# Kernel tuning notes

Measured on AMD Instinct MI355X. Metric: run time of the kernel, lower is better.

The kernel has to match this reference:

```python
import jax, jax.numpy as jnp
import numpy as np

N = 100000      # nodes
E = 1600000     # edges
F_IN = 64       # num_node_features
HID = 128       # hidden_channels
HEADS = 8       # heads in gat1
G = 1000        # number of graphs
EPS = 1e-5


def _layer_norm(x, gamma, beta):
    mu = jnp.mean(x, axis=-1, keepdims=True)
    var = jnp.var(x, axis=-1, keepdims=True)
    return (x - mu) * jax.lax.rsqrt(var + EPS) * gamma + beta


def _gat_conv(x, src, dst, W, a_src, a_dst, b):
    # PyG GATConv (concat=True, negative_slope=0.2, self-loops already in src/dst)
    n = x.shape[0]
    heads, c = a_src.shape
    h = (x @ W).reshape(n, heads, c)                      # [N,H,C]
    alpha_s = jnp.sum(h * a_src[None], axis=-1)           # [N,H]
    alpha_d = jnp.sum(h * a_dst[None], axis=-1)           # [N,H]
    e = jax.nn.leaky_relu(alpha_s[src] + alpha_d[dst], 0.2)   # [Etot,H]
    m = jax.ops.segment_max(e, dst, num_segments=n)       # per-dst max (stable softmax)
    e = jnp.exp(e - m[dst])
    denom = jax.ops.segment_sum(e, dst, num_segments=n)
    attn = e / (denom[dst] + 1e-16)                        # [Etot,H]
    out = jax.ops.segment_sum(h[src] * attn[:, :, None], dst, num_segments=n)
    return out.reshape(n, heads * c) + b


def setup_inputs():
    key = jax.random.key(0)
    ks = jax.random.split(key, 32)
    s = 0.05
    inp = {
        'x': jax.random.normal(ks[0], (N, F_IN), dtype=jnp.float32),
        'edge_index': jax.random.randint(ks[1], (2, E), 0, N),
        'batch': jnp.sort(jax.random.randint(ks[2], (N,), 0, G)),
        # gat1: 64 -> 16 per head, 8 heads
        'W1': jax.random.normal(ks[3], (F_IN, HID), dtype=jnp.float32) * s,
        'as1': jax.random.normal(ks[4], (HEADS, HID // HEADS), dtype=jnp.float32) * s,
        'ad1': jax.random.normal(ks[5], (HEADS, HID // HEADS), dtype=jnp.float32) * s,
        'b1': jnp.zeros((HID,), dtype=jnp.float32),
        # gat2: 128 -> 128, 1 head
        'W2': jax.random.normal(ks[6], (HID, HID), dtype=jnp.float32) * s,
        'as2': jax.random.normal(ks[7], (1, HID), dtype=jnp.float32) * s,
        'ad2': jax.random.normal(ks[8], (1, HID), dtype=jnp.float32) * s,
        'b2': jnp.zeros((HID,), dtype=jnp.float32),
        # gat3
        'W3': jax.random.normal(ks[9], (HID, HID), dtype=jnp.float32) * s,
        'as3': jax.random.normal(ks[10], (1, HID), dtype=jnp.float32) * s,
        'ad3': jax.random.normal(ks[11], (1, HID), dtype=jnp.float32) * s,
        'b3': jnp.zeros((HID,), dtype=jnp.float32),
        # layer norms
        'g1': jnp.ones((HID,), dtype=jnp.float32), 'be1': jnp.zeros((HID,), dtype=jnp.float32),
        'g2': jnp.ones((HID,), dtype=jnp.float32), 'be2': jnp.zeros((HID,), dtype=jnp.float32),
        'g3': jnp.ones((HID,), dtype=jnp.float32), 'be3': jnp.zeros((HID,), dtype=jnp.float32),
        # linear heads
        'lw1': jax.random.normal(ks[12], (HID, HID), dtype=jnp.float32) * s,
        'lb1': jnp.zeros((HID,), dtype=jnp.float32),
        'lw2': jax.random.normal(ks[13], (HID, HID), dtype=jnp.float32) * s,
        'lb2': jnp.zeros((HID,), dtype=jnp.float32),
    }
    return inp


def reference(x, edge_index, batch, W1, as1, ad1, b1, W2, as2, ad2, b2,
              W3, as3, ad3, b3, g1, be1, g2, be2, g3, be3, lw1, lb1, lw2, lb2):
    n = x.shape[0]
    loops = jnp.arange(n)
    src = jnp.concatenate([edge_index[0], loops])   # add self-loops (PyG default)
    dst = jnp.concatenate([edge_index[1], loops])

    h = _gat_conv(x, src, dst, W1, as1, ad1, b1)
    h = _layer_norm(jax.nn.elu(h), g1, be1)          # dropout is identity in eval

    idn2 = h
    h = _gat_conv(h, src, dst, W2, as2, ad2, b2)
    h = _layer_norm(jax.nn.elu(h), g2, be2) + idn2

    idn3 = h
    h = _gat_conv(h, src, dst, W3, as3, ad3, b3)
    h = _layer_norm(jax.nn.elu(h), g3, be3) + idn3

    # global mean pool over graphs
    sums = jax.ops.segment_sum(h, batch, num_segments=G)
    cnt = jax.ops.segment_sum(jnp.ones((n, 1), h.dtype), batch, num_segments=G)
    pooled = sums / jnp.maximum(cnt, 1.0)

    out = jax.nn.elu(pooled @ lw1 + lb1)
    return out @ lw2 + lb2
```

## Files before the change

kernel.cpp:

```cpp
#include <hip/hip_runtime.h>
#include <hip/hip_bf16.h>
#include <cstdint>
#include <cstddef>

constexpr int F_IN = 64;
constexpr int HID  = 128;
constexpr int SCHUNK = 4096;

typedef __attribute__((ext_vector_type(8))) short short8v;
typedef __attribute__((ext_vector_type(4))) float f32x4;

__device__ __forceinline__ float bf2f(unsigned short u) {
  return __uint_as_float((unsigned)u << 16);
}
__device__ __forceinline__ unsigned short f2bf(float x) {
  unsigned u = __float_as_uint(x);
  u += 0x7FFFu + ((u >> 16) & 1u);
  return (unsigned short)(u >> 16);
}

__global__ __launch_bounds__(256) void k_bhist(const int* __restrict__ ei,
                                               int* __restrict__ bcnt, int E, int n) {
  __shared__ int hist[1024];
  int t = threadIdx.x;
  for (int k = t; k < 1024; k += 256) hist[k] = 0;
  __syncthreads();
  int tot = E + n;
  for (int i = blockIdx.x * 256 + t; i < tot; i += gridDim.x * 256) {
    int d = (i < E) ? ei[E + i] : (i - E);
    atomicAdd(&hist[d >> 7], 1);
  }
  __syncthreads();
  for (int k = t; k < 1024; k += 256)
    if (hist[k]) atomicAdd(&bcnt[k], hist[k]);
}

__global__ __launch_bounds__(1024) void k_bscan(const int* __restrict__ bcnt,
                                                int* __restrict__ boff,
                                                int* __restrict__ bcur, int nb) {
  __shared__ int tmp[1024];
  int t = threadIdx.x;
  int v = (t < nb) ? bcnt[t] : 0;
  tmp[t] = v;
  __syncthreads();
  #pragma unroll
  for (int off = 1; off < 1024; off <<= 1) {
    int x = tmp[t];
    int add = (t >= off) ? tmp[t - off] : 0;
    __syncthreads();
    tmp[t] = x + add;
    __syncthreads();
  }
  if (t < nb) {
    int ex = tmp[t] - v;
    boff[t] = ex;
    bcur[t] = ex;
    if (t == nb - 1) boff[nb] = tmp[t];
  }
}

__global__ __launch_bounds__(256) void k_bscat(const int* __restrict__ ei,
                                               int* __restrict__ bcur,
                                               uint2* __restrict__ pairs, int E, int n) {
  __shared__ int lh[1024];
  __shared__ int lc[1024];
  int t = threadIdx.x;
  int tot = E + n;
  int start = blockIdx.x * SCHUNK;
  if (start >= tot) return;
  int end = min(start + SCHUNK, tot);
  for (int k = t; k < 1024; k += 256) { lh[k] = 0; lc[k] = 0; }
  __syncthreads();
  int dreg[SCHUNK / 256];
  #pragma unroll
  for (int q = 0; q < SCHUNK / 256; ++q) {
    int i = start + q * 256 + t;
    int d = (i < end) ? ((i < E) ? ei[E + i] : (i - E)) : -1;
    dreg[q] = d;
    if (d >= 0) atomicAdd(&lh[d >> 7], 1);
  }
  __syncthreads();
  for (int k = t; k < 1024; k += 256) {
    int c = lh[k];
    lh[k] = (c > 0) ? atomicAdd(&bcur[k], c) : 0;
  }
  __syncthreads();
  #pragma unroll
  for (int q = 0; q < SCHUNK / 256; ++q) {
    int i = start + q * 256 + t;
    int d = dreg[q];
    if (d < 0) continue;
    int s = (i < E) ? ei[i] : (i - E);
    int b = d >> 7;
    int loc = atomicAdd(&lc[b], 1);
    pairs[lh[b] + loc] = make_uint2((unsigned)s, (unsigned)d);
  }
}

__global__ __launch_bounds__(256) void k_bfin(const uint2* __restrict__ pairs,
                                              const int* __restrict__ boff,
                                              int* __restrict__ row_off,
                                              int* __restrict__ csr_src,
                                              int n, int tot) {
  __shared__ int ldeg[128];
  __shared__ int lcur[128];
  int b = blockIdx.x;
  int t = threadIdx.x;
  int pb = boff[b], pe = boff[b + 1];
  if (t < 128) ldeg[t] = 0;
  __syncthreads();
  for (int j = pb + t; j < pe; j += 256)
    atomicAdd(&ldeg[pairs[j].y & 127], 1);
  __syncthreads();
  int cnt = (t < 128) ? ldeg[t] : 0;
  for (int off = 1; off < 128; off <<= 1) {
    int add = (t < 128 && t >= off) ? ldeg[t - off] : 0;
    __syncthreads();
    if (t < 128) ldeg[t] += add;
    __syncthreads();
  }
  if (t < 128) {
    int base = pb + ldeg[t] - cnt;
    lcur[t] = base;
    int idx = (b << 7) + t;
    if (idx < n) row_off[idx] = base;
  }
  if (b == 0 && t == 255) row_off[n] = tot;
  __syncthreads();
  for (int j = pb + t; j < pe; j += 256) {
    uint2 pr = pairs[j];
    int pos = atomicAdd(&lcur[pr.y & 127], 1);
    csr_src[pos] = (int)pr.x;
  }
}

__global__ void k_tobf(const float* __restrict__ X, unsigned short* __restrict__ Y,
                       int total) {
  int i = blockIdx.x * 256 + threadIdx.x;
  if (i < total) Y[i] = f2bf(X[i]);
}

__global__ void k_wpack(const float* __restrict__ W, unsigned short* __restrict__ Wf,
                        int K) {
  int i = blockIdx.x * 256 + threadIdx.x;
  int total = (K >> 5) * 4096;
  if (i >= total) return;
  int j    = i & 7;
  int lane = (i >> 3) & 63;
  int t    = (i >> 9) & 7;
  int ks   = i >> 12;
  int k = ks * 32 + (lane >> 4) * 8 + j;
  int c = t * 16 + (lane & 15);
  Wf[i] = f2bf(W[k * 128 + c]);
}

template<int K>
__global__ __launch_bounds__(256) void k_mgemm(const short* __restrict__ Xb,
                                               const short* __restrict__ Wf,
                                               unsigned short* __restrict__ Y, int n) {
  int wv   = threadIdx.x >> 6;
  int lane = threadIdx.x & 63;
  int r0   = blockIdx.x * 64 + wv * 16;
  int ln = lane & 15, kg = lane >> 4;
  f32x4 acc[8] = {};
  int arow = min(r0 + ln, n - 1);
  const short* aptr = Xb + arow * K + kg * 8;
  #pragma unroll
  for (int ks = 0; ks < K / 32; ++ks) {
    short8v a = *(const short8v*)(aptr + ks * 32);
    const short* wp = Wf + ks * 4096 + lane * 8;
    #pragma unroll
    for (int t = 0; t < 8; ++t) {
      short8v b = *(const short8v*)(wp + t * 512);
      acc[t] = __builtin_amdgcn_mfma_f32_16x16x32_bf16(a, b, acc[t], 0, 0, 0);
    }
  }
  #pragma unroll
  for (int t = 0; t < 8; ++t) {
    #pragma unroll
    for (int reg = 0; reg < 4; ++reg) {
      int r = r0 + kg * 4 + reg;
      if (r < n) Y[r * 128 + t * 16 + ln] = f2bf(acc[t][reg]);
    }
  }
}

template<int LOGC>
__global__ __launch_bounds__(256) void k_alpha(const unsigned short* __restrict__ H,
    const float* __restrict__ a_s, const float* __restrict__ a_d,
    float* __restrict__ AS, float* __restrict__ AD, int n) {
  int wid  = (int)((blockIdx.x * (size_t)blockDim.x + threadIdx.x) >> 6);
  int lane = threadIdx.x & 63;
  if (wid >= n) return;
  constexpr int SEG = 1 << (LOGC - 1);
  constexpr int NH  = HID >> LOGC;
  int c = 2 * lane;
  ushort2 u = *(const ushort2*)(H + wid * HID + c);
  float h0 = bf2f(u.x), h1 = bf2f(u.y);
  float s1 = h0 * a_s[c] + h1 * a_s[c + 1];
  float s2 = h0 * a_d[c] + h1 * a_d[c + 1];
  #pragma unroll
  for (int off = 1; off < SEG; off <<= 1) {
    s1 += __shfl_xor(s1, off);
    s2 += __shfl_xor(s2, off);
  }
  if ((lane & (SEG - 1)) == 0) {
    int h = lane / SEG;
    AS[wid * NH + h] = s1;
    AD[wid * NH + h] = s2;
  }
}

template<int LOGC>
__global__ __launch_bounds__(256) void k_agg_post(const unsigned short* __restrict__ Hu,
    const int* __restrict__ row_off, const int* __restrict__ csr_src,
    const float* __restrict__ AS, const float* __restrict__ AD,
    const float* __restrict__ bias, const float* __restrict__ RES,
    const float* __restrict__ gamma, const float* __restrict__ beta,
    float* __restrict__ Y, unsigned short* __restrict__ Yb, int n, int has_res) {
  int tid = blockIdx.x * 256 + threadIdx.x;
  int wid = tid >> 5;
  int ll  = threadIdx.x & 31;
  if (wid >= n) return;
  constexpr int NH  = HID >> LOGC;
  constexpr int SEG = (LOGC >= 7) ? 32 : (1 << (LOGC - 2));
  int abslane = threadIdx.x & 63;
  int c = ll << 2;
  int h = c >> LOGC;
  int r = ll & (SEG - 1);
  int sbase = abslane & ~(SEG - 1);
  float adv = AD[wid * NH + h];
  int jb = row_off[wid], je = row_off[wid + 1];
  float den = 0.f, a0 = 0.f, a1 = 0.f, a2 = 0.f, a3 = 0.f;
  for (int j0 = jb; j0 < je; j0 += SEG) {
    int cnt = min(SEG, je - j0);
    int s_l = 0; float p_l = 0.f;
    if (r < cnt) {
      s_l = csr_src[j0 + r];
      float e = AS[s_l * NH + h] + adv;
      e = (e > 0.f) ? e : 0.2f * e;
      p_l = __expf(e);
    }
    int k = 0;
    for (; k + 4 <= cnt; k += 4) {
      int sk0 = __shfl(s_l, sbase | k);
      int sk1 = __shfl(s_l, sbase | (k + 1));
      int sk2 = __shfl(s_l, sbase | (k + 2));
      int sk3 = __shfl(s_l, sbase | (k + 3));
      ushort4 u0 = *(const ushort4*)(Hu + (sk0 << 7) + c);
      ushort4 u1 = *(const ushort4*)(Hu + (sk1 << 7) + c);
      ushort4 u2 = *(const ushort4*)(Hu + (sk2 << 7) + c);
      ushort4 u3 = *(const ushort4*)(Hu + (sk3 << 7) + c);
      float p0 = __shfl(p_l, sbase | k);
      float p1 = __shfl(p_l, sbase | (k + 1));
      float p2 = __shfl(p_l, sbase | (k + 2));
      float p3 = __shfl(p_l, sbase | (k + 3));
      den += (p0 + p1) + (p2 + p3);
      a0 = fmaf(p0, bf2f(u0.x), a0); a1 = fmaf(p0, bf2f(u0.y), a1);
      a2 = fmaf(p0, bf2f(u0.z), a2); a3 = fmaf(p0, bf2f(u0.w), a3);
      a0 = fmaf(p1, bf2f(u1.x), a0); a1 = fmaf(p1, bf2f(u1.y), a1);
      a2 = fmaf(p1, bf2f(u1.z), a2); a3 = fmaf(p1, bf2f(u1.w), a3);
      a0 = fmaf(p2, bf2f(u2.x), a0); a1 = fmaf(p2, bf2f(u2.y), a1);
      a2 = fmaf(p2, bf2f(u2.z), a2); a3 = fmaf(p2, bf2f(u2.w), a3);
      a0 = fmaf(p3, bf2f(u3.x), a0); a1 = fmaf(p3, bf2f(u3.y), a1);
      a2 = fmaf(p3, bf2f(u3.z), a2); a3 = fmaf(p3, bf2f(u3.w), a3);
    }
    for (; k < cnt; ++k) {
      int   s  = __shfl(s_l, sbase | k);
      float pk = __shfl(p_l, sbase | k);
      ushort4 u = *(const ushort4*)(Hu + (s << 7) + c);
      den += pk;
      a0 = fmaf(pk, bf2f(u.x), a0); a1 = fmaf(pk, bf2f(u.y), a1);
      a2 = fmaf(pk, bf2f(u.z), a2); a3 = fmaf(pk, bf2f(u.w), a3);
    }
  }
  float inv = 1.f / (den + 1e-16f);
  float4 bv = *(const float4*)(bias + c);
  float t0 = a0 * inv + bv.x;
  float t1 = a1 * inv + bv.y;
  float t2 = a2 * inv + bv.z;
  float t3 = a3 * inv + bv.w;
  float e0 = t0 > 0.f ? t0 : __expf(t0) - 1.f;
  float e1 = t1 > 0.f ? t1 : __expf(t1) - 1.f;
  float e2 = t2 > 0.f ? t2 : __expf(t2) - 1.f;
  float e3 = t3 > 0.f ? t3 : __expf(t3) - 1.f;
  float s1 = (e0 + e1) + (e2 + e3);
  float s2 = (e0 * e0 + e1 * e1) + (e2 * e2 + e3 * e3);
  #pragma unroll
  for (int off = 16; off >= 1; off >>= 1) {
    s1 += __shfl_xor(s1, off);
    s2 += __shfl_xor(s2, off);
  }
  float mu  = s1 * (1.f / 128.f);
  float var = s2 * (1.f / 128.f) - mu * mu;
  float rs  = rsqrtf(var + 1e-5f);
  int base = wid * HID;
  float4 rv = make_float4(0.f, 0.f, 0.f, 0.f);
  if (has_res) rv = *(const float4*)(RES + base + c);
  float4 gv = *(const float4*)(gamma + c);
  float4 betv = *(const float4*)(beta + c);
  float4 o;
  o.x = (e0 - mu) * rs * gv.x + betv.x + rv.x;
  o.y = (e1 - mu) * rs * gv.y + betv.y + rv.y;
  o.z = (e2 - mu) * rs * gv.z + betv.z + rv.z;
  o.w = (e3 - mu) * rs * gv.w + betv.w + rv.w;
  *(float4*)(Y + base + c) = o;
  if (Yb) {
    ushort4 ob;
    ob.x = f2bf(o.x);
    ob.y = f2bf(o.y);
    ob.z = f2bf(o.z);
    ob.w = f2bf(o.w);
    *(ushort4*)(Yb + base + c) = ob;
  }
}

__global__ __launch_bounds__(256) void k_pool_seg(const float* __restrict__ Hf,
    const int* __restrict__ batch, float* __restrict__ pool, int n, int G) {
  int wid  = (int)((blockIdx.x * (size_t)blockDim.x + threadIdx.x) >> 6);
  int lane = threadIdx.x & 63;
  if (wid >= G) return;
  int lo = 0, hi = n;
  while (lo < hi) { int mid = (lo + hi) >> 1; if (batch[mid] < wid) lo = mid + 1; else hi = mid; }
  int start = lo;
  hi = n;
  while (lo < hi) { int mid = (lo + hi) >> 1; if (batch[mid] < wid + 1) lo = mid + 1; else hi = mid; }
  int end = lo;
  int c = 2 * lane;
  float s0 = 0.f, s1 = 0.f;
  for (int i = start; i < end; ++i) {
    float2 v = *(const float2*)(Hf + (size_t)i * HID + c);
    s0 += v.x; s1 += v.y;
  }
  float inv = 1.f / (float)max(end - start, 1);
  pool[(size_t)wid * HID + c]     = s0 * inv;
  pool[(size_t)wid * HID + c + 1] = s1 * inv;
}

__global__ void k_mlp(const float* __restrict__ X, const float* __restrict__ Wt,
                      const float* __restrict__ bb, float* __restrict__ Y,
                      int rows, int do_elu) {
  int i = blockIdx.x * blockDim.x + threadIdx.x;
  if (i >= rows * HID) return;
  int r = i >> 7, c = i & 127;
  const float* xr = X + (size_t)r * HID;
  float acc = bb[c];
  for (int k = 0; k < HID; ++k) acc += xr[k] * Wt[k * HID + c];
  if (do_elu) acc = acc > 0.f ? acc : __expf(acc) - 1.f;
  Y[i] = acc;
}

extern "C" void kernel_launch(void* const* d_in, const int* in_sizes, int n_in,
                              void* d_out, int out_size, void* d_ws, size_t ws_size,
                              hipStream_t stream) {
  const float* x   = (const float*)d_in[0];
  const int*   ei  = (const int*)d_in[1];
  const int*   bat = (const int*)d_in[2];
  const float* W1  = (const float*)d_in[3];
  const float* as1 = (const float*)d_in[4];
  const float* ad1 = (const float*)d_in[5];
  const float* b1  = (const float*)d_in[6];
  const float* W2  = (const float*)d_in[7];
  const float* as2 = (const float*)d_in[8];
  const float* ad2 = (const float*)d_in[9];
  const float* b2  = (const float*)d_in[10];
  const float* W3  = (const float*)d_in[11];
  const float* as3 = (const float*)d_in[12];
  const float* ad3 = (const float*)d_in[13];
  const float* b3  = (const float*)d_in[14];
  const float* g1  = (const float*)d_in[15];
  const float* be1 = (const float*)d_in[16];
  const float* g2  = (const float*)d_in[17];
  const float* be2 = (const float*)d_in[18];
  const float* g3  = (const float*)d_in[19];
  const float* be3 = (const float*)d_in[20];
  const float* lw1 = (const float*)d_in[21];
  const float* lb1 = (const float*)d_in[22];
  const float* lw2 = (const float*)d_in[23];
  const float* lb2 = (const float*)d_in[24];

  int N = in_sizes[0] / F_IN;
  int E = in_sizes[1] / 2;
  int G = out_size / HID;
  int tot = E + N;
  int nb  = (N + 127) >> 7;

  char* p = (char*)d_ws;
  auto alloc = [&](size_t bytes) { char* r = p; p += (bytes + 511) & ~(size_t)511; return r; };
  int*   bcnt    = (int*)  alloc(1024 * 4);
  int*   boff    = (int*)  alloc(1025 * 4);
  int*   bcur    = (int*)  alloc(1024 * 4);
  int*   row_off = (int*)  alloc((size_t)(N + 1) * 4);
  int*   csr_src = (int*)  alloc((size_t)tot * 4);
  uint2* pairs   = (uint2*)alloc((size_t)tot * 8);
  float* AS      = (float*)alloc((size_t)N * 8 * 4);
  float* AD      = (float*)alloc((size_t)N * 8 * 4);
  unsigned short* Hb  = (unsigned short*)alloc((size_t)N * HID * 2);
  unsigned short* Fb  = (unsigned short*)alloc((size_t)N * HID * 2);
  float* F0      = (float*)alloc((size_t)N * HID * 4);
  float* F1      = (float*)alloc((size_t)N * HID * 4);
  float* pool    = (float*)alloc((size_t)G * HID * 4);
  float* t1      = (float*)alloc((size_t)G * HID * 4);
  unsigned short* Wf1 = (unsigned short*)alloc(64 * 128 * 2);
  unsigned short* Wf2 = (unsigned short*)alloc(128 * 128 * 2);
  unsigned short* Wf3 = (unsigned short*)alloc(128 * 128 * 2);
  unsigned short* xb  = (unsigned short*)pairs;

  (void)hipMemsetAsync(bcnt, 0, 1024 * 4, stream);

  int sb = (tot + SCHUNK - 1) / SCHUNK;
  k_bhist<<<256, 256, 0, stream>>>(ei, bcnt, E, N);
  k_bscan<<<1, 1024, 0, stream>>>(bcnt, boff, bcur, nb);
  k_bscat<<<sb, 256, 0, stream>>>(ei, bcur, pairs, E, N);
  k_bfin <<<nb, 256, 0, stream>>>(pairs, boff, row_off, csr_src, N, tot);

  k_tobf <<<(N * F_IN + 255) / 256, 256, 0, stream>>>(x, xb, N * F_IN);
  k_wpack<<<(64 * 128 + 255) / 256, 256, 0, stream>>>(W1, Wf1, 64);
  k_wpack<<<(128 * 128 + 255) / 256, 256, 0, stream>>>(W2, Wf2, 128);
  k_wpack<<<(128 * 128 + 255) / 256, 256, 0, stream>>>(W3, Wf3, 128);

  int mb  = (N + 63) / 64;
  int nw  = (N + 3) / 4;
  int nh2 = (N + 7) / 8;

  k_mgemm<64><<<mb, 256, 0, stream>>>((const short*)xb, (const short*)Wf1, Hb, N);
  k_alpha<4><<<nw, 256, 0, stream>>>(Hb, as1, ad1, AS, AD, N);
  k_agg_post<4><<<nh2, 256, 0, stream>>>(Hb, row_off, csr_src, AS, AD, b1,
                                         nullptr, g1, be1, F0, Fb, N, 0);

  k_mgemm<128><<<mb, 256, 0, stream>>>((const short*)Fb, (const short*)Wf2, Hb, N);
  k_alpha<7><<<nw, 256, 0, stream>>>(Hb, as2, ad2, AS, AD, N);
  k_agg_post<7><<<nh2, 256, 0, stream>>>(Hb, row_off, csr_src, AS, AD, b2,
                                         F0, g2, be2, F1, Fb, N, 1);

  k_mgemm<128><<<mb, 256, 0, stream>>>((const short*)Fb, (const short*)Wf3, Hb, N);
  k_alpha<7><<<nw, 256, 0, stream>>>(Hb, as3, ad3, AS, AD, N);
  k_agg_post<7><<<nh2, 256, 0, stream>>>(Hb, row_off, csr_src, AS, AD, b3,
                                         F1, g3, be3, F0, nullptr, N, 1);

  k_pool_seg<<<(G + 3) / 4, 256, 0, stream>>>(F0, bat, pool, N, G);
  k_mlp<<<(G * HID + 255) / 256, 256, 0, stream>>>(pool, lw1, lb1, t1, G, 1);
  k_mlp<<<(G * HID + 255) / 256, 256, 0, stream>>>(t1, lw2, lb2, (float*)d_out, G, 0);
}
```

Before: 468.4 us.

## Fuse attention logits into GEMM, store activations as bf16, unroll aggregation by 8

The attention-coefficient dot products (alpha_src/alpha_dst) are now computed in the MFMA GEMM epilogue from the fp32 accumulators, which removes the separate k_alpha kernels and their re-read of H. Layer outputs, residuals and the pooling input are stored only as bf16 instead of both fp32 and bf16, cutting memory traffic in aggregation and pooling. The single-head aggregation loop also issues 8 gathers at a time to get more loads in flight. The trade-off is lower residual precision from bf16 storage and more register pressure in the GEMM epilogue and aggregation loop.

```diff
diff --git a/kernel.cpp b/kernel.cpp
--- a/kernel.cpp
+++ b/kernel.cpp
@@ -154,10 +154,14 @@
   Wf[i] = f2bf(W[k * 128 + c]);
 }
 
-template<int K>
+template<int K, int HEADS>
 __global__ __launch_bounds__(256) void k_mgemm(const short* __restrict__ Xb,
                                                const short* __restrict__ Wf,
-                                               unsigned short* __restrict__ Y, int n) {
+                                               const float* __restrict__ a_s,
+                                               const float* __restrict__ a_d,
+                                               unsigned short* __restrict__ Y,
+                                               float* __restrict__ AS,
+                                               float* __restrict__ AD, int n) {
   int wv   = threadIdx.x >> 6;
   int lane = threadIdx.x & 63;
   int r0   = blockIdx.x * 64 + wv * 16;
@@ -175,6 +179,50 @@
       acc[t] = __builtin_amdgcn_mfma_f32_16x16x32_bf16(a, b, acc[t], 0, 0, 0);
     }
   }
+  float asv[8], adv[8];
+  #pragma unroll
+  for (int t = 0; t < 8; ++t) { asv[t] = a_s[t * 16 + ln]; adv[t] = a_d[t * 16 + ln]; }
+  #pragma unroll
+  for (int reg = 0; reg < 4; ++reg) {
+    int r = r0 + kg * 4 + reg;
+    bool valid = (r < n);
+    if (HEADS == 1) {
+      float s1 = 0.f, s2 = 0.f;
+      #pragma unroll
+      for (int t = 0; t < 8; ++t) {
+        s1 = fmaf(acc[t][reg], asv[t], s1);
+        s2 = fmaf(acc[t][reg], adv[t], s2);
+      }
+      #pragma unroll
+      for (int off = 1; off < 16; off <<= 1) {
+        s1 += __shfl_xor(s1, off);
+        s2 += __shfl_xor(s2, off);
+      }
+      if (valid && ln == 0) { AS[r] = s1; AD[r] = s2; }
+    } else {
+      float s1[8], s2[8];
+      #pragma unroll
+      for (int t = 0; t < 8; ++t) {
+        s1[t] = acc[t][reg] * asv[t];
+        s2[t] = acc[t][reg] * adv[t];
+      }
+      #pragma unroll
+      for (int off = 1; off < 16; off <<= 1) {
+        #pragma unroll
+        for (int t = 0; t < 8; ++t) {
+          s1[t] += __shfl_xor(s1[t], off);
+          s2[t] += __shfl_xor(s2[t], off);
+        }
+      }
+      float w1 = s1[0], w2 = s2[0];
+      #pragma unroll
+      for (int t = 1; t < 8; ++t) {
+        w1 = (ln == t) ? s1[t] : w1;
+        w2 = (ln == t) ? s2[t] : w2;
+      }
+      if (valid && ln < 8) { AS[r * 8 + ln] = w1; AD[r * 8 + ln] = w2; }
+    }
+  }
   #pragma unroll
   for (int t = 0; t < 8; ++t) {
     #pragma unroll
@@ -186,38 +234,12 @@
 }
 
 template<int LOGC>
-__global__ __launch_bounds__(256) void k_alpha(const unsigned short* __restrict__ H,
-    const float* __restrict__ a_s, const float* __restrict__ a_d,
-    float* __restrict__ AS, float* __restrict__ AD, int n) {
-  int wid  = (int)((blockIdx.x * (size_t)blockDim.x + threadIdx.x) >> 6);
-  int lane = threadIdx.x & 63;
-  if (wid >= n) return;
-  constexpr int SEG = 1 << (LOGC - 1);
-  constexpr int NH  = HID >> LOGC;
-  int c = 2 * lane;
-  ushort2 u = *(const ushort2*)(H + wid * HID + c);
-  float h0 = bf2f(u.x), h1 = bf2f(u.y);
-  float s1 = h0 * a_s[c] + h1 * a_s[c + 1];
-  float s2 = h0 * a_d[c] + h1 * a_d[c + 1];
-  #pragma unroll
-  for (int off = 1; off < SEG; off <<= 1) {
-    s1 += __shfl_xor(s1, off);
-    s2 += __shfl_xor(s2, off);
-  }
-  if ((lane & (SEG - 1)) == 0) {
-    int h = lane / SEG;
-    AS[wid * NH + h] = s1;
-    AD[wid * NH + h] = s2;
-  }
-}
-
-template<int LOGC>
 __global__ __launch_bounds__(256) void k_agg_post(const unsigned short* __restrict__ Hu,
     const int* __restrict__ row_off, const int* __restrict__ csr_src,
     const float* __restrict__ AS, const float* __restrict__ AD,
-    const float* __restrict__ bias, const float* __restrict__ RES,
+    const float* __restrict__ bias, const unsigned short* __restrict__ RES,
     const float* __restrict__ gamma, const float* __restrict__ beta,
-    float* __restrict__ Y, unsigned short* __restrict__ Yb, int n, int has_res) {
+    unsigned short* __restrict__ Yb, int n, int has_res) {
   int tid = blockIdx.x * 256 + threadIdx.x;
   int wid = tid >> 5;
   int ll  = threadIdx.x & 31;
@@ -242,6 +264,25 @@
       p_l = __expf(e);
     }
     int k = 0;
+    if (LOGC >= 7) {
+      for (; k + 8 <= cnt; k += 8) {
+        int   sk[8]; float pk[8]; ushort4 uu[8];
+        #pragma unroll
+        for (int q = 0; q < 8; ++q) sk[q] = __shfl(s_l, sbase | (k + q));
+        #pragma unroll
+        for (int q = 0; q < 8; ++q) uu[q] = *(const ushort4*)(Hu + (sk[q] << 7) + c);
+        #pragma unroll
+        for (int q = 0; q < 8; ++q) pk[q] = __shfl(p_l, sbase | (k + q));
+        #pragma unroll
+        for (int q = 0; q < 8; ++q) {
+          den += pk[q];
+          a0 = fmaf(pk[q], bf2f(uu[q].x), a0);
+          a1 = fmaf(pk[q], bf2f(uu[q].y), a1);
+          a2 = fmaf(pk[q], bf2f(uu[q].z), a2);
+          a3 = fmaf(pk[q], bf2f(uu[q].w), a3);
+        }
+      }
+    }
     for (; k + 4 <= cnt; k += 4) {
       int sk0 = __shfl(s_l, sbase | k);
       int sk1 = __shfl(s_l, sbase | (k + 1));
@@ -295,27 +336,22 @@
   float var = s2 * (1.f / 128.f) - mu * mu;
   float rs  = rsqrtf(var + 1e-5f);
   int base = wid * HID;
-  float4 rv = make_float4(0.f, 0.f, 0.f, 0.f);
-  if (has_res) rv = *(const float4*)(RES + base + c);
+  float r0 = 0.f, r1 = 0.f, r2 = 0.f, r3 = 0.f;
+  if (has_res) {
+    ushort4 rv = *(const ushort4*)(RES + base + c);
+    r0 = bf2f(rv.x); r1 = bf2f(rv.y); r2 = bf2f(rv.z); r3 = bf2f(rv.w);
+  }
   float4 gv = *(const float4*)(gamma + c);
   float4 betv = *(const float4*)(beta + c);
-  float4 o;
-  o.x = (e0 - mu) * rs * gv.x + betv.x + rv.x;
-  o.y = (e1 - mu) * rs * gv.y + betv.y + rv.y;
-  o.z = (e2 - mu) * rs * gv.z + betv.z + rv.z;
-  o.w = (e3 - mu) * rs * gv.w + betv.w + rv.w;
-  *(float4*)(Y + base + c) = o;
-  if (Yb) {
-    ushort4 ob;
-    ob.x = f2bf(o.x);
-    ob.y = f2bf(o.y);
-    ob.z = f2bf(o.z);
-    ob.w = f2bf(o.w);
-    *(ushort4*)(Yb + base + c) = ob;
-  }
-}
-
-__global__ __launch_bounds__(256) void k_pool_seg(const float* __restrict__ Hf,
+  ushort4 ob;
+  ob.x = f2bf((e0 - mu) * rs * gv.x + betv.x + r0);
+  ob.y = f2bf((e1 - mu) * rs * gv.y + betv.y + r1);
+  ob.z = f2bf((e2 - mu) * rs * gv.z + betv.z + r2);
+  ob.w = f2bf((e3 - mu) * rs * gv.w + betv.w + r3);
+  *(ushort4*)(Yb + base + c) = ob;
+}
+
+__global__ __launch_bounds__(256) void k_pool_seg(const unsigned short* __restrict__ Hf,
     const int* __restrict__ batch, float* __restrict__ pool, int n, int G) {
   int wid  = (int)((blockIdx.x * (size_t)blockDim.x + threadIdx.x) >> 6);
   int lane = threadIdx.x & 63;
@@ -329,8 +365,8 @@
   int c = 2 * lane;
   float s0 = 0.f, s1 = 0.f;
   for (int i = start; i < end; ++i) {
-    float2 v = *(const float2*)(Hf + (size_t)i * HID + c);
-    s0 += v.x; s1 += v.y;
+    ushort2 v = *(const ushort2*)(Hf + (size_t)i * HID + c);
+    s0 += bf2f(v.x); s1 += bf2f(v.y);
   }
   float inv = 1.f / (float)max(end - start, 1);
   pool[(size_t)wid * HID + c]     = s0 * inv;
@@ -396,9 +432,9 @@
   float* AS      = (float*)alloc((size_t)N * 8 * 4);
   float* AD      = (float*)alloc((size_t)N * 8 * 4);
   unsigned short* Hb  = (unsigned short*)alloc((size_t)N * HID * 2);
-  unsigned short* Fb  = (unsigned short*)alloc((size_t)N * HID * 2);
-  float* F0      = (float*)alloc((size_t)N * HID * 4);
-  float* F1      = (float*)alloc((size_t)N * HID * 4);
+  unsigned short* Fb0 = (unsigned short*)alloc((size_t)N * HID * 2);
+  unsigned short* Fb1 = (unsigned short*)alloc((size_t)N * HID * 2);
+  unsigned short* Fb2 = (unsigned short*)alloc((size_t)N * HID * 2);
   float* pool    = (float*)alloc((size_t)G * HID * 4);
   float* t1      = (float*)alloc((size_t)G * HID * 4);
   unsigned short* Wf1 = (unsigned short*)alloc(64 * 128 * 2);
@@ -420,25 +456,24 @@
   k_wpack<<<(128 * 128 + 255) / 256, 256, 0, stream>>>(W3, Wf3, 128);
 
   int mb  = (N + 63) / 64;
-  int nw  = (N + 3) / 4;
   int nh2 = (N + 7) / 8;
 
-  k_mgemm<64><<<mb, 256, 0, stream>>>((const short*)xb, (const short*)Wf1, Hb, N);
-  k_alpha<4><<<nw, 256, 0, stream>>>(Hb, as1, ad1, AS, AD, N);
+  k_mgemm<64, 8><<<mb, 256, 0, stream>>>((const short*)xb, (const short*)Wf1,
+                                         as1, ad1, Hb, AS, AD, N);
   k_agg_post<4><<<nh2, 256, 0, stream>>>(Hb, row_off, csr_src, AS, AD, b1,
-                                         nullptr, g1, be1, F0, Fb, N, 0);
-
-  k_mgemm<128><<<mb, 256, 0, stream>>>((const short*)Fb, (const short*)Wf2, Hb, N);
-  k_alpha<7><<<nw, 256, 0, stream>>>(Hb, as2, ad2, AS, AD, N);
+                                         nullptr, g1, be1, Fb0, N, 0);
+
+  k_mgemm<128, 1><<<mb, 256, 0, stream>>>((const short*)Fb0, (const short*)Wf2,
+                                          as2, ad2, Hb, AS, AD, N);
   k_agg_post<7><<<nh2, 256, 0, stream>>>(Hb, row_off, csr_src, AS, AD, b2,
-                                         F0, g2, be2, F1, Fb, N, 1);
-
-  k_mgemm<128><<<mb, 256, 0, stream>>>((const short*)Fb, (const short*)Wf3, Hb, N);
-  k_alpha<7><<<nw, 256, 0, stream>>>(Hb, as3, ad3, AS, AD, N);
+                                         Fb0, g2, be2, Fb1, N, 1);
+
+  k_mgemm<128, 1><<<mb, 256, 0, stream>>>((const short*)Fb1, (const short*)Wf3,
+                                          as3, ad3, Hb, AS, AD, N);
   k_agg_post<7><<<nh2, 256, 0, stream>>>(Hb, row_off, csr_src, AS, AD, b3,
-                                         F1, g3, be3, F0, nullptr, N, 1);
-
-  k_pool_seg<<<(G + 3) / 4, 256, 0, stream>>>(F0, bat, pool, N, G);
+                                         Fb1, g3, be3, Fb2, N, 1);
+
+  k_pool_seg<<<(G + 3) / 4, 256, 0, stream>>>(Fb2, bat, pool, N, G);
   k_mlp<<<(G * HID + 255) / 256, 256, 0, stream>>>(pool, lw1, lb1, t1, G, 1);
   k_mlp<<<(G * HID + 255) / 256, 256, 0, stream>>>(t1, lw2, lb2, (float*)d_out, G, 0);
 }
```

After: 420.0 us. 10.3% less time.
